# Kernel tuning notes

Measured on AMD Instinct MI355X. Metric: run time of the kernel, lower is better.

The kernel has to match this reference:

```python
import jax, jax.numpy as jnp
import numpy as np

HEADS = 4

def _topk_mask(attn, k):
    # exact replica of mask.scatter_(-1, topk_indices, 1.0): exactly k ones per row
    C = attn.shape[-1]
    _, idx = jax.lax.top_k(attn, k)                      # [b,h,C,k]
    return jax.nn.one_hot(idx, C, dtype=attn.dtype).sum(axis=-2) > 0  # [b,h,C,C] bool


def setup_inputs() -> dict:
    key = jax.random.key(0)
    ks = jax.random.split(key, 8)
    b, dim, h, w = 32, 128, 4096, 1
    s = 0.05
    return {
        "x": jax.random.normal(ks[0], (b, dim, h, w), jnp.float32),
        "qkv_w": jax.random.normal(ks[1], (3 * dim, dim), jnp.float32) * s,
        "qkv_b": jax.random.normal(ks[2], (3 * dim,), jnp.float32) * s,
        "dw_w": jax.random.normal(ks[3], (3 * dim, 1, 3, 3), jnp.float32) * s,
        "dw_b": jax.random.normal(ks[4], (3 * dim,), jnp.float32) * s,
        "proj_w": jax.random.normal(ks[5], (dim, dim), jnp.float32) * s,
        "proj_b": jax.random.normal(ks[6], (dim,), jnp.float32) * s,
        "temperature": jnp.ones((HEADS, 1, 1), jnp.float32),
        "attn_w": jnp.full((4,), 0.2, jnp.float32),  # attn1..attn4
    }


def reference(x, qkv_w, qkv_b, dw_w, dw_b, proj_w, proj_b, temperature, attn_w):
    b, c, h, w = x.shape
    # 1x1 conv qkv, then 3x3 depthwise conv (groups = 3*c)
    qkv = jnp.einsum('bchw,oc->bohw', x, qkv_w) + qkv_b[None, :, None, None]
    qkv = jax.lax.conv_general_dilated(
        qkv, dw_w, window_strides=(1, 1), padding=((1, 1), (1, 1)),
        dimension_numbers=('NCHW', 'OIHW', 'NCHW'), feature_group_count=3 * c
    ) + dw_b[None, :, None, None]
    q, k, v = jnp.split(qkv, 3, axis=1)
    heads = lambda t: t.reshape(b, HEADS, c // HEADS, h * w)  # b head c (hw)
    q, k, v = heads(q), heads(k), heads(v)
    # F.normalize(dim=-1), eps=1e-12
    q = q / jnp.maximum(jnp.linalg.norm(q, axis=-1, keepdims=True), 1e-12)
    k = k / jnp.maximum(jnp.linalg.norm(k, axis=-1, keepdims=True), 1e-12)
    C = c // HEADS
    attn = jnp.einsum('bhcn,bhdn->bhcd', q, k) * temperature[None]  # [b,head,C,C]
    top_ks = [C // 2, (2 * C) // 3, (3 * C) // 4, (4 * C) // 5]
    out = jnp.zeros_like(v)
    for i, kk in enumerate(top_ks):
        m = _topk_mask(attn, kk)
        a = jax.nn.softmax(jnp.where(m, attn, -jnp.inf), axis=-1)
        out = out + attn_w[i] * jnp.einsum('bhcd,bhdn->bhcn', a, v)
    out = out.reshape(b, c, h, w)
    out = jnp.einsum('bchw,oc->bohw', out, proj_w) + proj_b[None, :, None, None]
    return out
```

## Files before the change

kernel.cpp:

```cpp
#include <hip/hip_runtime.h>

#define B_ 32
#define CD 128
#define O3 384
#define N  4096
#define H_ 4
#define C_ 32

typedef __bf16 bf16x8 __attribute__((ext_vector_type(8)));
typedef float floatx4 __attribute__((ext_vector_type(4)));

#define MFMA16(a, b, c) __builtin_amdgcn_mfma_f32_16x16x32_bf16(a, b, c, 0, 0, 0)

__device__ __forceinline__ unsigned short f2b(float f) {
  unsigned int bits = __builtin_bit_cast(unsigned int, f);
  unsigned int r = (bits + 0x7FFFu + ((bits >> 16) & 1u)) >> 16;
  return (unsigned short)r;
}

__global__ __launch_bounds__(256) void k0_xt(const float* __restrict__ x,
                                             unsigned short* __restrict__ xT)
{
  __shared__ float xt[32 * 68];
  const int t = threadIdx.x;
  const int n0 = blockIdx.x * 64, c0 = blockIdx.y * 32, b = blockIdx.z;
  const float* xb = x + ((size_t)b * CD + c0) * N + n0;
#pragma unroll
  for (int i = 0; i < 2; i++) {
    int f = i * 256 + t;
    int c = f >> 4, n4 = (f & 15) * 4;
    float4 v = *(const float4*)(xb + (size_t)c * N + n4);
    *(float4*)&xt[c * 68 + n4] = v;
  }
  __syncthreads();
  int n = t >> 2, cb = (t & 3) * 8;
  unsigned short tmp[8];
#pragma unroll
  for (int j = 0; j < 8; j++) tmp[j] = f2b(xt[(cb + j) * 68 + n]);
  *(uint4*)(xT + ((size_t)b * N + n0 + n) * CD + c0 + cb) = *(uint4*)tmp;
}

__global__ void k0_w(const float* __restrict__ qkv_w,
                     const float* __restrict__ proj_w,
                     unsigned short* __restrict__ qkv_wb,
                     unsigned short* __restrict__ proj_wb)
{
  int e = (blockIdx.x * 256 + threadIdx.x) * 4;
  const float* src; unsigned short* dst; int off;
  if (e < 49152) { src = qkv_w; dst = qkv_wb; off = e; }
  else           { src = proj_w; dst = proj_wb; off = e - 49152; }
  float4 v = *(const float4*)(src + off);
  unsigned short tmp[4] = {f2b(v.x), f2b(v.y), f2b(v.z), f2b(v.w)};
  *(uint2*)(dst + off) = *(uint2*)tmp;
}

__global__ __launch_bounds__(256) void k1_qkv_dw(
    const unsigned short* __restrict__ xT, const unsigned short* __restrict__ qkv_wb,
    const float* __restrict__ qkv_b, const float* __restrict__ dw_w,
    const float* __restrict__ dw_b, unsigned short* __restrict__ qkvd,
    unsigned short* __restrict__ vT)
{
  __shared__ __align__(16) char smem[69632];
  unsigned short* As = (unsigned short*)smem;
  unsigned short* Bs = (unsigned short*)(smem + 34816);
  float* pres = (float*)smem;

  const int t = threadIdx.x;
  const int ytile = blockIdx.x, otile = blockIdx.y, b = blockIdx.z;
  const int obase = otile * 128;
  const int ybase = ytile * 126 - 1;
  const int wv = t >> 6, l = t & 63, quad = l >> 4, lm = l & 15;

#pragma unroll
  for (int i = 0; i < 8; i++) {
    int f = i * 256 + t;
    int o = f >> 4, c8 = (f & 15) * 8;
    *(uint4*)&As[o * 136 + c8] =
        *(const uint4*)(qkv_wb + (size_t)(obase + o) * CD + c8);
  }
#pragma unroll
  for (int i = 0; i < 8; i++) {
    int f = i * 256 + t;
    int row = f >> 4, c8 = (f & 15) * 8;
    int yg = ybase + row;
    uint4 v = make_uint4(0u, 0u, 0u, 0u);
    if (yg >= 0 && yg < N)
      v = *(const uint4*)(xT + ((size_t)b * N + yg) * CD + c8);
    *(uint4*)&Bs[row * 136 + c8] = v;
  }
  __syncthreads();

  floatx4 acc[2][8];
#pragma unroll
  for (int mt = 0; mt < 2; mt++)
#pragma unroll
    for (int nt = 0; nt < 8; nt++) acc[mt][nt] = (floatx4){0.f, 0.f, 0.f, 0.f};

#pragma unroll
  for (int ks = 0; ks < 4; ks++) {
    int k0 = ks * 32 + quad * 8;
    bf16x8 a0 = *(const bf16x8*)&As[(wv * 32 + lm) * 136 + k0];
    bf16x8 a1 = *(const bf16x8*)&As[(wv * 32 + 16 + lm) * 136 + k0];
#pragma unroll
    for (int nt = 0; nt < 8; nt++) {
      bf16x8 bb = *(const bf16x8*)&Bs[(nt * 16 + lm) * 136 + k0];
      acc[0][nt] = MFMA16(a0, bb, acc[0][nt]);
      acc[1][nt] = MFMA16(a1, bb, acc[1][nt]);
    }
  }
  __syncthreads();

  if (otile < 2) {
#pragma unroll
    for (int mt = 0; mt < 2; mt++)
#pragma unroll
      for (int r = 0; r < 4; r++) {
        int o = wv * 32 + mt * 16 + quad * 4 + r;
        float bias = qkv_b[obase + o];
#pragma unroll
        for (int nt = 0; nt < 8; nt++) {
          int y = nt * 16 + lm;
          int yg = ybase + y;
          pres[o * 130 + y] = (yg >= 0 && yg < N) ? (acc[mt][nt][r] + bias) : 0.f;
        }
      }
    __syncthreads();
    const int y2 = t & 127, og = t >> 7;
    int yo = ybase + y2;
    bool ok = (y2 >= 1) && (y2 <= 126) && (yo < N);
    for (int r = 0; r < 64; r++) {
      int o = og * 64 + r;
      int oo = obase + o;
      float v = dw_w[oo * 9 + 1] * pres[o * 130 + y2 - 1] +
                dw_w[oo * 9 + 4] * pres[o * 130 + y2] +
                dw_w[oo * 9 + 7] * pres[o * 130 + y2 + 1] + dw_b[oo];
      if (ok) qkvd[((size_t)b * 256 + oo) * N + yo] = f2b(v);
    }
  } else {
#pragma unroll
    for (int mt = 0; mt < 2; mt++)
#pragma unroll
      for (int r = 0; r < 4; r++) {
        int o = wv * 32 + mt * 16 + quad * 4 + r;
        float bias = qkv_b[obase + o];
#pragma unroll
        for (int nt = 0; nt < 8; nt++) {
          int y = nt * 16 + lm;
          int yg = ybase + y;
          pres[y * 131 + o] = (yg >= 0 && yg < N) ? (acc[mt][nt][r] + bias) : 0.f;
        }
      }
    __syncthreads();
    const int o = t & 127, half = t >> 7;
    const int oo = obase + o;
    const float w0 = dw_w[oo * 9 + 1], w1 = dw_w[oo * 9 + 4],
                w2 = dw_w[oo * 9 + 7], wb = dw_b[oo];
    int ys = 1 + half * 63;
    float pm = pres[(ys - 1) * 131 + o];
    float pc = pres[ys * 131 + o];
    for (int yy = ys; yy < ys + 63; yy++) {
      float pp = pres[(yy + 1) * 131 + o];
      int yo2 = ybase + yy;
      if (yo2 < N) {
        float v = w0 * pm + w1 * pc + w2 * pp + wb;
        vT[((size_t)b * N + yo2) * CD + o] = f2b(v);
      }
      pm = pc; pc = pp;
    }
  }
}

__global__ __launch_bounds__(256) void k3_gram(
    const unsigned short* __restrict__ qkvd, float* __restrict__ part)
{
  __shared__ unsigned short Qs[32 * 136];
  __shared__ unsigned short Ks[32 * 136];
  __shared__ float red[4 * 8 * 272];
  const int ns = blockIdx.x, h = blockIdx.y, b = blockIdx.z;
  const int t = threadIdx.x;
  const int wv = t >> 6, l = t & 63, quad = l >> 4, lm = l & 15;
  const unsigned short* qb = qkvd + ((size_t)b * 256 + h * C_) * N;
  const unsigned short* kb = qkvd + ((size_t)b * 256 + 128 + h * C_) * N;
  const int n0 = ns * 1024;

  floatx4 acc[8];
#pragma unroll
  for (int i = 0; i < 8; i++) acc[i] = (floatx4){0.f, 0.f, 0.f, 0.f};

  for (int ch = 0; ch < 8; ch++) {
    int nc = n0 + ch * 128;
#pragma unroll
    for (int i = 0; i < 4; i++) {
      int f = i * 256 + t;
      int row = f >> 4, n8 = (f & 15) * 8;
      const unsigned short* src = (row < 32) ? (qb + (size_t)row * N)
                                             : (kb + (size_t)(row - 32) * N);
      uint4 u = *(const uint4*)(src + nc + n8);
      unsigned short* dst = (row < 32) ? &Qs[row * 136 + n8]
                                       : &Ks[(row - 32) * 136 + n8];
      *(uint4*)dst = u;
    }
    __syncthreads();
    int k0 = wv * 32 + quad * 8;
    bf16x8 a0 = *(const bf16x8*)&Qs[lm * 136 + k0];
    bf16x8 a1 = *(const bf16x8*)&Qs[(16 + lm) * 136 + k0];
    bf16x8 b0 = *(const bf16x8*)&Ks[lm * 136 + k0];
    bf16x8 b1 = *(const bf16x8*)&Ks[(16 + lm) * 136 + k0];
    acc[0] = MFMA16(a0, b0, acc[0]);
    acc[1] = MFMA16(a0, b1, acc[1]);
    acc[2] = MFMA16(a1, b0, acc[2]);
    acc[3] = MFMA16(a1, b1, acc[3]);
    acc[4] = MFMA16(a0, a0, acc[4]);
    acc[5] = MFMA16(a1, a1, acc[5]);
    acc[6] = MFMA16(b0, b0, acc[6]);
    acc[7] = MFMA16(b1, b1, acc[7]);
    __syncthreads();
  }

#pragma unroll
  for (int tl = 0; tl < 8; tl++)
#pragma unroll
    for (int r = 0; r < 4; r++)
      red[wv * 2176 + tl * 272 + (quad * 4 + r) * 17 + lm] = acc[tl][r];
  __syncthreads();

  float* pb = part + ((size_t)(b * H_ + h) * 4 + ns) * 2048;
  for (int e = t; e < 2048; e += 256) {
    int tl = e >> 8, rc = e & 255, row = rc >> 4, col = rc & 15;
    int a = tl * 272 + row * 17 + col;
    float s = red[a] + red[2176 + a] + red[2 * 2176 + a] + red[3 * 2176 + a];
    if (tl < 4) {
      int mt = tl >> 1, nt = tl & 1;
      pb[(mt * 16 + row) * 32 + nt * 16 + col] = s;
    } else if (row == col) {
      if (tl < 6) pb[1024 + (tl - 4) * 16 + row] = s;
      else        pb[1056 + (tl - 6) * 16 + row] = s;
    }
  }
}

__global__ __launch_bounds__(256) void k45(
    const float* __restrict__ part, const unsigned short* __restrict__ proj_wb,
    const float* __restrict__ temperature, const float* __restrict__ attn_w,
    unsigned short* __restrict__ Mb)
{
  __shared__ float La[H_][C_][33];
  __shared__ float sq2[256];
  __shared__ float rn[256];
  __shared__ float exL[H_][C_][33];
  __shared__ unsigned char rkL[H_][C_][C_];
  __shared__ unsigned short AwtT[H_][C_][40];
  const int b = blockIdx.x, t = threadIdx.x;

  const float* pbb = part + (size_t)b * 32768;
  for (int e = t; e < 4 * 2048; e += 256) {
    int h = e >> 11, idx = e & 2047;
    if (idx < 1088) {
      const float* p = pbb + h * 8192 + idx;
      float s = p[0] + p[2048] + p[2 * 2048] + p[3 * 2048];
      if (idx < 1024) La[h][idx >> 5][idx & 31] = s;
      else if (idx < 1056) sq2[h * 32 + (idx - 1024)] = s;
      else sq2[128 + h * 32 + (idx - 1056)] = s;
    }
  }
  __syncthreads();
  rn[t] = 1.f / fmaxf(sqrtf(sq2[t]), 1e-12f);
  __syncthreads();
  for (int e = t; e < 4096; e += 256) {
    int h = e >> 10, i = (e >> 5) & 31, j = e & 31;
    La[h][i][j] *= rn[h * 32 + i] * rn[128 + h * 32 + j] * temperature[h];
  }
  __syncthreads();

  if (t < 128) {
    int h = t >> 5, i = t & 31;
    float m = -1e30f;
    for (int j = 0; j < 32; j++) m = fmaxf(m, La[h][i][j]);
    float S0 = 0.f, S1 = 0.f, S2 = 0.f, S3 = 0.f;
    for (int j = 0; j < 32; j++) {
      float vj = La[h][i][j];
      int r = 0;
      for (int j2 = 0; j2 < 32; j2++) {
        float v2 = La[h][i][j2];
        r += (v2 > vj) || (v2 == vj && j2 < j);
      }
      float e = __expf(vj - m);
      exL[h][i][j] = e;
      rkL[h][i][j] = (unsigned char)r;
      if (r < 16) S0 += e;
      if (r < 21) S1 += e;
      if (r < 24) S2 += e;
      if (r < 25) S3 += e;
    }
    float w0 = attn_w[0] / S0, w1 = attn_w[1] / S1;
    float w2 = attn_w[2] / S2, w3 = attn_w[3] / S3;
    for (int j = 0; j < 32; j++) {
      int r = rkL[h][i][j];
      float cmb = (r < 16 ? w0 : 0.f) + (r < 21 ? w1 : 0.f) +
                  (r < 24 ? w2 : 0.f) + (r < 25 ? w3 : 0.f);
      AwtT[h][j][i] = f2b(exL[h][i][j] * cmb);
    }
  }
  __syncthreads();

  {
    const int wv = t >> 6, l = t & 63, quad = l >> 4, lm = l & 15;
    const int h = wv;
    bf16x8 bfr[2];
#pragma unroll
    for (int jt = 0; jt < 2; jt++)
      bfr[jt] = *(const bf16x8*)&AwtT[h][jt * 16 + lm][quad * 8];
#pragma unroll
    for (int mt = 0; mt < 8; mt++) {
      bf16x8 a = *(const bf16x8*)(proj_wb +
                    (size_t)(mt * 16 + lm) * CD + h * C_ + quad * 8);
#pragma unroll
      for (int jt = 0; jt < 2; jt++) {
        floatx4 acc = (floatx4){0.f, 0.f, 0.f, 0.f};
        acc = MFMA16(a, bfr[jt], acc);
#pragma unroll
        for (int r = 0; r < 4; r++) {
          int row = quad * 4 + r;
          Mb[(size_t)b * 16384 + (mt * 16 + row) * CD + h * C_ + jt * 16 + lm] =
              f2b(acc[r]);
        }
      }
    }
  }
}

__global__ __launch_bounds__(256) void k6_out(
    const unsigned short* __restrict__ vT, const unsigned short* __restrict__ Mb,
    const float* __restrict__ proj_b, float* __restrict__ out)
{
  __shared__ unsigned short As[128 * 136];
  __shared__ unsigned short Bs[128 * 136];
  const int t = threadIdx.x;
  const int y0 = blockIdx.x * 128, b = blockIdx.y;
  const int wv = t >> 6, l = t & 63, quad = l >> 4, lm = l & 15;

#pragma unroll
  for (int i = 0; i < 8; i++) {
    int f = i * 256 + t;
    int o = f >> 4, c8 = (f & 15) * 8;
    *(uint4*)&As[o * 136 + c8] =
        *(const uint4*)(Mb + ((size_t)b * CD + o) * CD + c8);
  }
#pragma unroll
  for (int i = 0; i < 8; i++) {
    int f = i * 256 + t;
    int row = f >> 4, c8 = (f & 15) * 8;
    *(uint4*)&Bs[row * 136 + c8] =
        *(const uint4*)(vT + ((size_t)b * N + y0 + row) * CD + c8);
  }
  __syncthreads();

  floatx4 acc[2][8];
#pragma unroll
  for (int mt = 0; mt < 2; mt++)
#pragma unroll
    for (int nt = 0; nt < 8; nt++) acc[mt][nt] = (floatx4){0.f, 0.f, 0.f, 0.f};

#pragma unroll
  for (int ks = 0; ks < 4; ks++) {
    int k0 = ks * 32 + quad * 8;
    bf16x8 a0 = *(const bf16x8*)&As[(wv * 32 + lm) * 136 + k0];
    bf16x8 a1 = *(const bf16x8*)&As[(wv * 32 + 16 + lm) * 136 + k0];
#pragma unroll
    for (int nt = 0; nt < 8; nt++) {
      bf16x8 bb = *(const bf16x8*)&Bs[(nt * 16 + lm) * 136 + k0];
      acc[0][nt] = MFMA16(a0, bb, acc[0][nt]);
      acc[1][nt] = MFMA16(a1, bb, acc[1][nt]);
    }
  }

#pragma unroll
  for (int mt = 0; mt < 2; mt++)
#pragma unroll
    for (int r = 0; r < 4; r++) {
      int o = wv * 32 + mt * 16 + quad * 4 + r;
      float pb = proj_b[o];
#pragma unroll
      for (int nt = 0; nt < 8; nt++) {
        int y = y0 + nt * 16 + lm;
        out[((size_t)b * CD + o) * N + y] = acc[mt][nt][r] + pb;
      }
    }
}

extern "C" void kernel_launch(void* const* d_in, const int* in_sizes, int n_in,
                              void* d_out, int out_size, void* d_ws, size_t ws_size,
                              hipStream_t stream)
{
  (void)in_sizes; (void)n_in; (void)out_size; (void)ws_size;
  const float* x           = (const float*)d_in[0];
  const float* qkv_w       = (const float*)d_in[1];
  const float* qkv_b       = (const float*)d_in[2];
  const float* dw_w        = (const float*)d_in[3];
  const float* dw_b        = (const float*)d_in[4];
  const float* proj_w      = (const float*)d_in[5];
  const float* proj_b      = (const float*)d_in[6];
  const float* temperature = (const float*)d_in[7];
  const float* attn_w      = (const float*)d_in[8];
  float* out = (float*)d_out;

  unsigned short* xT      = (unsigned short*)d_ws;
  unsigned short* qkv_wb  = xT + (size_t)16777216;
  unsigned short* proj_wb = qkv_wb + 49152;
  unsigned short* qkvd    = proj_wb + 16384;
  unsigned short* vT      = qkvd + (size_t)33554432;
  unsigned short* Mb      = vT + (size_t)16777216;
  float* part = (float*)(Mb + 524288);

  k0_xt    <<<dim3(64, 4, 32),  256, 0, stream>>>(x, xT);
  k0_w     <<<dim3(64),         256, 0, stream>>>(qkv_w, proj_w, qkv_wb, proj_wb);
  k1_qkv_dw<<<dim3(33, 3, 32),  256, 0, stream>>>(xT, qkv_wb, qkv_b, dw_w, dw_b,
                                                  qkvd, vT);
  k3_gram  <<<dim3(4, H_, B_),  256, 0, stream>>>(qkvd, part);
  k45      <<<dim3(B_),         256, 0, stream>>>(part, proj_wb, temperature,
                                                  attn_w, Mb);
  k6_out   <<<dim3(32, B_),     256, 0, stream>>>(vT, Mb, proj_b, out);
}
```

Baseline: 291.8 us.

## Shrink LDS use: load weights directly from global, bf16 staging, drop gram LDS

The qkv and output GEMM kernels now read their A operand (weights or Mb) straight from global memory into MFMA registers instead of staging it in shared memory, halving LDS per block. The depthwise-conv staging buffer is stored as bf16 rather than fp32, and the q/k path processes two outputs per thread with packed 32-bit stores. The gram kernel drops its shared-memory tiles and barriers and loads fragments directly from global. Together with launch_bounds(256,4) and a retiled y-range, this aims to raise occupancy and remove sync and LDS traffic. The cost is uncoalesced global fragment loads and an extra bf16 rounding of the pre-conv activations.

```diff
diff --git a/kernel.cpp b/kernel.cpp
--- a/kernel.cpp
+++ b/kernel.cpp
@@ -12,6 +12,12 @@
 
 #define MFMA16(a, b, c) __builtin_amdgcn_mfma_f32_16x16x32_bf16(a, b, c, 0, 0, 0)
 
+__device__ __forceinline__ float b2f(unsigned int u) {
+  return __builtin_bit_cast(float, u << 16);
+}
+__device__ __forceinline__ float b2fh(unsigned int u) {
+  return __builtin_bit_cast(float, u & 0xffff0000u);
+}
 __device__ __forceinline__ unsigned short f2b(float f) {
   unsigned int bits = __builtin_bit_cast(unsigned int, f);
   unsigned int r = (bits + 0x7FFFu + ((bits >> 16) & 1u)) >> 16;
@@ -54,35 +60,27 @@
   *(uint2*)(dst + off) = *(uint2*)tmp;
 }
 
-__global__ __launch_bounds__(256) void k1_qkv_dw(
+__global__ __launch_bounds__(256, 4) void k1_qkv_dw(
     const unsigned short* __restrict__ xT, const unsigned short* __restrict__ qkv_wb,
     const float* __restrict__ qkv_b, const float* __restrict__ dw_w,
     const float* __restrict__ dw_b, unsigned short* __restrict__ qkvd,
     unsigned short* __restrict__ vT)
 {
-  __shared__ __align__(16) char smem[69632];
-  unsigned short* As = (unsigned short*)smem;
-  unsigned short* Bs = (unsigned short*)(smem + 34816);
-  float* pres = (float*)smem;
+  __shared__ __align__(16) char smem[34816];
+  unsigned short* Bs   = (unsigned short*)smem;
+  unsigned short* pres = (unsigned short*)smem;
 
   const int t = threadIdx.x;
   const int ytile = blockIdx.x, otile = blockIdx.y, b = blockIdx.z;
   const int obase = otile * 128;
-  const int ybase = ytile * 126 - 1;
+  const int ybase = ytile * 124;
   const int wv = t >> 6, l = t & 63, quad = l >> 4, lm = l & 15;
 
-#pragma unroll
-  for (int i = 0; i < 8; i++) {
-    int f = i * 256 + t;
-    int o = f >> 4, c8 = (f & 15) * 8;
-    *(uint4*)&As[o * 136 + c8] =
-        *(const uint4*)(qkv_wb + (size_t)(obase + o) * CD + c8);
-  }
 #pragma unroll
   for (int i = 0; i < 8; i++) {
     int f = i * 256 + t;
     int row = f >> 4, c8 = (f & 15) * 8;
-    int yg = ybase + row;
+    int yg = ybase - 2 + row;
     uint4 v = make_uint4(0u, 0u, 0u, 0u);
     if (yg >= 0 && yg < N)
       v = *(const uint4*)(xT + ((size_t)b * N + yg) * CD + c8);
@@ -96,21 +94,22 @@
 #pragma unroll
     for (int nt = 0; nt < 8; nt++) acc[mt][nt] = (floatx4){0.f, 0.f, 0.f, 0.f};
 
+  const unsigned short* wbase =
+      qkv_wb + (size_t)(obase + wv * 32 + lm) * CD + quad * 8;
 #pragma unroll
   for (int ks = 0; ks < 4; ks++) {
-    int k0 = ks * 32 + quad * 8;
-    bf16x8 a0 = *(const bf16x8*)&As[(wv * 32 + lm) * 136 + k0];
-    bf16x8 a1 = *(const bf16x8*)&As[(wv * 32 + 16 + lm) * 136 + k0];
+    bf16x8 a0 = *(const bf16x8*)(wbase + ks * 32);
+    bf16x8 a1 = *(const bf16x8*)(wbase + 16 * CD + ks * 32);
 #pragma unroll
     for (int nt = 0; nt < 8; nt++) {
-      bf16x8 bb = *(const bf16x8*)&Bs[(nt * 16 + lm) * 136 + k0];
+      bf16x8 bb = *(const bf16x8*)&Bs[(nt * 16 + lm) * 136 + ks * 32 + quad * 8];
       acc[0][nt] = MFMA16(a0, bb, acc[0][nt]);
       acc[1][nt] = MFMA16(a1, bb, acc[1][nt]);
     }
   }
-  __syncthreads();
 
   if (otile < 2) {
+    __syncthreads();
 #pragma unroll
     for (int mt = 0; mt < 2; mt++)
 #pragma unroll
@@ -119,93 +118,91 @@
         float bias = qkv_b[obase + o];
 #pragma unroll
         for (int nt = 0; nt < 8; nt++) {
-          int y = nt * 16 + lm;
-          int yg = ybase + y;
-          pres[o * 130 + y] = (yg >= 0 && yg < N) ? (acc[mt][nt][r] + bias) : 0.f;
+          int i = nt * 16 + lm;
+          if (i >= 1) {
+            int yg = ybase - 2 + i;
+            pres[o * 132 + (i - 1)] =
+                f2b((yg >= 0 && yg < N) ? (acc[mt][nt][r] + bias) : 0.f);
+          }
         }
       }
     __syncthreads();
-    const int y2 = t & 127, og = t >> 7;
-    int yo = ybase + y2;
-    bool ok = (y2 >= 1) && (y2 <= 126) && (yo < N);
-    for (int r = 0; r < 64; r++) {
-      int o = og * 64 + r;
-      int oo = obase + o;
-      float v = dw_w[oo * 9 + 1] * pres[o * 130 + y2 - 1] +
-                dw_w[oo * 9 + 4] * pres[o * 130 + y2] +
-                dw_w[oo * 9 + 7] * pres[o * 130 + y2 + 1] + dw_b[oo];
-      if (ok) qkvd[((size_t)b * 256 + oo) * N + yo] = f2b(v);
+    const int p = t & 63, og = t >> 6;
+    const bool ok = (p < 62) && (ybase + 2 * p < N);
+    const unsigned int* presu = (const unsigned int*)pres;
+    for (int r2 = 0; r2 < 32; r2++) {
+      int oo = __builtin_amdgcn_readfirstlane(obase + og * 32 + r2);
+      float w0 = dw_w[oo * 9 + 1], w1 = dw_w[oo * 9 + 4],
+            w2 = dw_w[oo * 9 + 7], db = dw_b[oo];
+      int o = oo - obase;
+      unsigned int u0 = presu[(o * 132 >> 1) + p];
+      unsigned int u1 = presu[(o * 132 >> 1) + p + 1];
+      float v0 = b2f(u0), v1 = b2fh(u0), v2 = b2f(u1), v3 = b2fh(u1);
+      float out0 = w0 * v0 + w1 * v1 + w2 * v2 + db;
+      float out1 = w0 * v1 + w1 * v2 + w2 * v3 + db;
+      unsigned int pk = (unsigned int)f2b(out0) |
+                        ((unsigned int)f2b(out1) << 16);
+      if (ok)
+        *(unsigned int*)(qkvd + ((size_t)b * 256 + oo) * N + ybase + 2 * p) = pk;
     }
   } else {
-#pragma unroll
-    for (int mt = 0; mt < 2; mt++)
-#pragma unroll
-      for (int r = 0; r < 4; r++) {
-        int o = wv * 32 + mt * 16 + quad * 4 + r;
-        float bias = qkv_b[obase + o];
-#pragma unroll
-        for (int nt = 0; nt < 8; nt++) {
-          int y = nt * 16 + lm;
-          int yg = ybase + y;
-          pres[y * 131 + o] = (yg >= 0 && yg < N) ? (acc[mt][nt][r] + bias) : 0.f;
-        }
-      }
-    __syncthreads();
     const int o = t & 127, half = t >> 7;
     const int oo = obase + o;
     const float w0 = dw_w[oo * 9 + 1], w1 = dw_w[oo * 9 + 4],
-                w2 = dw_w[oo * 9 + 7], wb = dw_b[oo];
-    int ys = 1 + half * 63;
-    float pm = pres[(ys - 1) * 131 + o];
-    float pc = pres[ys * 131 + o];
-    for (int yy = ys; yy < ys + 63; yy++) {
-      float pp = pres[(yy + 1) * 131 + o];
-      int yo2 = ybase + yy;
-      if (yo2 < N) {
-        float v = w0 * pm + w1 * pc + w2 * pp + wb;
-        vT[((size_t)b * N + yo2) * CD + o] = f2b(v);
+                w2 = dw_w[oo * 9 + 7], db = dw_b[oo];
+    __syncthreads();
+#pragma unroll
+    for (int mt = 0; mt < 2; mt++)
+#pragma unroll
+      for (int r = 0; r < 4; r++) {
+        int o2 = wv * 32 + mt * 16 + quad * 4 + r;
+        float bias = qkv_b[obase + o2];
+#pragma unroll
+        for (int nt = 0; nt < 8; nt++) {
+          int i = nt * 16 + lm;
+          int yg = ybase - 2 + i;
+          pres[i * 132 + o2] =
+              f2b((yg >= 0 && yg < N) ? (acc[mt][nt][r] + bias) : 0.f);
+        }
+      }
+    __syncthreads();
+    int i0 = 2 + half * 62;
+    float pm = b2f((unsigned int)pres[(i0 - 1) * 132 + o]);
+    float pc = b2f((unsigned int)pres[i0 * 132 + o]);
+    for (int i = i0; i < i0 + 62; i++) {
+      float pp = b2f((unsigned int)pres[(i + 1) * 132 + o]);
+      int yo = ybase - 2 + i;
+      if (yo < N) {
+        float v = w0 * pm + w1 * pc + w2 * pp + db;
+        vT[((size_t)b * N + yo) * CD + o] = f2b(v);
       }
       pm = pc; pc = pp;
     }
   }
 }
 
-__global__ __launch_bounds__(256) void k3_gram(
+__global__ __launch_bounds__(256, 4) void k3_gram(
     const unsigned short* __restrict__ qkvd, float* __restrict__ part)
 {
-  __shared__ unsigned short Qs[32 * 136];
-  __shared__ unsigned short Ks[32 * 136];
   __shared__ float red[4 * 8 * 272];
   const int ns = blockIdx.x, h = blockIdx.y, b = blockIdx.z;
   const int t = threadIdx.x;
   const int wv = t >> 6, l = t & 63, quad = l >> 4, lm = l & 15;
   const unsigned short* qb = qkvd + ((size_t)b * 256 + h * C_) * N;
   const unsigned short* kb = qkvd + ((size_t)b * 256 + 128 + h * C_) * N;
-  const int n0 = ns * 1024;
 
   floatx4 acc[8];
 #pragma unroll
   for (int i = 0; i < 8; i++) acc[i] = (floatx4){0.f, 0.f, 0.f, 0.f};
 
+  const int nbase = ns * 1024 + wv * 32 + quad * 8;
+#pragma unroll
   for (int ch = 0; ch < 8; ch++) {
-    int nc = n0 + ch * 128;
-#pragma unroll
-    for (int i = 0; i < 4; i++) {
-      int f = i * 256 + t;
-      int row = f >> 4, n8 = (f & 15) * 8;
-      const unsigned short* src = (row < 32) ? (qb + (size_t)row * N)
-                                             : (kb + (size_t)(row - 32) * N);
-      uint4 u = *(const uint4*)(src + nc + n8);
-      unsigned short* dst = (row < 32) ? &Qs[row * 136 + n8]
-                                       : &Ks[(row - 32) * 136 + n8];
-      *(uint4*)dst = u;
-    }
-    __syncthreads();
-    int k0 = wv * 32 + quad * 8;
-    bf16x8 a0 = *(const bf16x8*)&Qs[lm * 136 + k0];
-    bf16x8 a1 = *(const bf16x8*)&Qs[(16 + lm) * 136 + k0];
-    bf16x8 b0 = *(const bf16x8*)&Ks[lm * 136 + k0];
-    bf16x8 b1 = *(const bf16x8*)&Ks[(16 + lm) * 136 + k0];
+    int nc = nbase + ch * 128;
+    bf16x8 a0 = *(const bf16x8*)(qb + (size_t)lm * N + nc);
+    bf16x8 a1 = *(const bf16x8*)(qb + (size_t)(16 + lm) * N + nc);
+    bf16x8 b0 = *(const bf16x8*)(kb + (size_t)lm * N + nc);
+    bf16x8 b1 = *(const bf16x8*)(kb + (size_t)(16 + lm) * N + nc);
     acc[0] = MFMA16(a0, b0, acc[0]);
     acc[1] = MFMA16(a0, b1, acc[1]);
     acc[2] = MFMA16(a1, b0, acc[2]);
@@ -214,7 +211,6 @@
     acc[5] = MFMA16(a1, a1, acc[5]);
     acc[6] = MFMA16(b0, b0, acc[6]);
     acc[7] = MFMA16(b1, b1, acc[7]);
-    __syncthreads();
   }
 
 #pragma unroll
@@ -329,23 +325,15 @@
   }
 }
 
-__global__ __launch_bounds__(256) void k6_out(
+__global__ __launch_bounds__(256, 4) void k6_out(
     const unsigned short* __restrict__ vT, const unsigned short* __restrict__ Mb,
     const float* __restrict__ proj_b, float* __restrict__ out)
 {
-  __shared__ unsigned short As[128 * 136];
   __shared__ unsigned short Bs[128 * 136];
   const int t = threadIdx.x;
   const int y0 = blockIdx.x * 128, b = blockIdx.y;
   const int wv = t >> 6, l = t & 63, quad = l >> 4, lm = l & 15;
 
-#pragma unroll
-  for (int i = 0; i < 8; i++) {
-    int f = i * 256 + t;
-    int o = f >> 4, c8 = (f & 15) * 8;
-    *(uint4*)&As[o * 136 + c8] =
-        *(const uint4*)(Mb + ((size_t)b * CD + o) * CD + c8);
-  }
 #pragma unroll
   for (int i = 0; i < 8; i++) {
     int f = i * 256 + t;
@@ -361,14 +349,15 @@
 #pragma unroll
     for (int nt = 0; nt < 8; nt++) acc[mt][nt] = (floatx4){0.f, 0.f, 0.f, 0.f};
 
+  const unsigned short* mbase =
+      Mb + (size_t)b * 16384 + (size_t)(wv * 32 + lm) * CD + quad * 8;
 #pragma unroll
   for (int ks = 0; ks < 4; ks++) {
-    int k0 = ks * 32 + quad * 8;
-    bf16x8 a0 = *(const bf16x8*)&As[(wv * 32 + lm) * 136 + k0];
-    bf16x8 a1 = *(const bf16x8*)&As[(wv * 32 + 16 + lm) * 136 + k0];
+    bf16x8 a0 = *(const bf16x8*)(mbase + ks * 32);
+    bf16x8 a1 = *(const bf16x8*)(mbase + 16 * CD + ks * 32);
 #pragma unroll
     for (int nt = 0; nt < 8; nt++) {
-      bf16x8 bb = *(const bf16x8*)&Bs[(nt * 16 + lm) * 136 + k0];
+      bf16x8 bb = *(const bf16x8*)&Bs[(nt * 16 + lm) * 136 + ks * 32 + quad * 8];
       acc[0][nt] = MFMA16(a0, bb, acc[0][nt]);
       acc[1][nt] = MFMA16(a1, bb, acc[1][nt]);
     }
@@ -414,7 +403,7 @@
 
   k0_xt    <<<dim3(64, 4, 32),  256, 0, stream>>>(x, xT);
   k0_w     <<<dim3(64),         256, 0, stream>>>(qkv_w, proj_w, qkv_wb, proj_wb);
-  k1_qkv_dw<<<dim3(33, 3, 32),  256, 0, stream>>>(xT, qkv_wb, qkv_b, dw_w, dw_b,
+  k1_qkv_dw<<<dim3(34, 3, 32),  256, 0, stream>>>(xT, qkv_wb, qkv_b, dw_w, dw_b,
                                                   qkvd, vT);
   k3_gram  <<<dim3(4, H_, B_),  256, 0, stream>>>(qkvd, part);
   k45      <<<dim3(B_),         256, 0, stream>>>(part, proj_wb, temperature,
```

Result: faster. 269.7 us (-7.6%).
